# Performance work log

Hardware: AMD Instinct MI355X
Metric: run time of the kernel (lower is better)

The kernel has to match this reference:

```python
import jax, jax.numpy as jnp
import numpy as np

N_NODES = 100000
N_EDGES = 3200000
N_TYPES = 4
SIGMA = 0.05


def setup_inputs() -> dict:
    key = jax.random.key(0)
    k1, k2, k3, k4 = jax.random.split(key, 4)
    pos = jax.random.uniform(k1, (N_NODES, 2), dtype=jnp.float32)
    # per-type attraction-repulsion parameters (p0..p3), kept positive-ish
    p = jax.random.uniform(k2, (N_TYPES, 4), dtype=jnp.float32) + 0.2
    cell_type = jax.random.randint(k3, (N_NODES,), 0, N_TYPES, dtype=jnp.int32)
    edge_index = jax.random.randint(k4, (2, N_EDGES), 0, N_NODES, dtype=jnp.int32)
    # func_type[n] % 2 == 0 -> 'arbitrary' (f1), == 1 -> 'tanh' (f2)
    func_type = jnp.arange(N_TYPES, dtype=jnp.int32)
    return {"pos": pos, "p": p, "cell_type": cell_type,
            "edge_index": edge_index, "func_type": func_type}


def reference(pos, p, cell_type, edge_index, func_type):
    n_cells = pos.shape[0]
    inv_2s2 = 1.0 / (2.0 * SIGMA * SIGMA)

    src, dst = edge_index[1], edge_index[0]
    valid = src != dst  # remove_self_loops, done via masking for static shapes

    dpos = pos[src] - pos[dst]                  # [E, 2] bc_dpos = identity
    d2 = jnp.sum(dpos * dpos, axis=1)           # [E]
    d2 = jnp.where(valid, d2, 1.0)              # guard pow/sqrt/div at self-loops
    dist = jnp.sqrt(d2)

    params = p[cell_type[dst]]                  # [E, 4] gather per dst node type
    p0, p1, p2, p3 = params[:, 0], params[:, 1], params[:, 2], params[:, 3]

    # 'arbitrary' attraction-repulsion force
    f1 = p0 * jnp.exp(-(d2 ** p1) * inv_2s2) - p2 * jnp.exp(-(d2 ** p3) * inv_2s2)
    # 'tanh' force
    f2 = p0 * jnp.tanh((dist - p1) * p2) / dist

    is_tanh = (func_type[cell_type[dst]] % 2) == 1
    coef = jnp.where(is_tanh, f2, f1)           # [E]
    msg = coef[:, None] * dpos                  # field_j = 1 (has_field=False)
    msg = jnp.where(valid[:, None], msg, 0.0)

    sums = jax.ops.segment_sum(msg, dst, num_segments=n_cells)              # [N, 2]
    counts = jax.ops.segment_sum(valid.astype(pos.dtype), dst, num_segments=n_cells)
    return sums / jnp.maximum(counts, 1.0)[:, None]  # mean aggregation
```

## Files before the change

### kernel.cpp

```cpp
#include <hip/hip_runtime.h>

#define N_NODES 100000
#define N_EDGES 3200000

#define BLOCK   256
#define BLOCKB  512
#define WPB     8
#define NBLK    1280
#define EB      (N_EDGES / NBLK)
#define KAIT    10
#define KATAIL  (EB - 9 * BLOCK)
#define CSHIFT  11
#define CHUNK   2048
#define NCHUNK  49
#define CAP     128
#define BPC     16
#define BACT    (NCHUNK * BPC)
#define NSEG    (NBLK / BPC)
#define SRC_BITS 17
#define SRC_MASK ((1u << SRC_BITS) - 1)

#define FP_SCALE 131072.0f
#define FP_BIAS  (1 << 18)
#define FLD_MASK ((1u << 26) - 1)

__device__ __forceinline__ float edge_coef(float d2, float4 pp, int ct) {
    if (ct & 1) {
        const float dist = sqrtf(d2);
        const float x = (dist - pp.y) * pp.z;
        const float e = __expf(2.0f * x);
        const float t = (e - 1.0f) / (e + 1.0f);
        return pp.x * t / dist;
    }
    const float l = __logf(d2);
    const float a = __expf(pp.y * l);
    const float b = __expf(pp.w * l);
    return pp.x * __expf(-200.0f * a) - pp.z * __expf(-200.0f * b);
}

__global__ __launch_bounds__(BLOCK) void kA_scatter(
    const int* __restrict__ edge_index,
    unsigned int* __restrict__ bucket,
    unsigned int* __restrict__ cnts)
{
    __shared__ unsigned int cnt[NCHUNK];
    __shared__ unsigned int offs[NCHUNK];
    __shared__ unsigned int cur[NCHUNK];
    __shared__ unsigned int ordered[EB];
    const int g = blockIdx.x, tid = threadIdx.x;
    const int lane = tid & 63, wid = tid >> 6;
    if (tid < NCHUNK) cnt[tid] = 0u;
    __syncthreads();
    const int* __restrict__ dstRow = edge_index;
    const int* __restrict__ srcRow = edge_index + N_EDGES;
    const int e0 = g * EB + tid;
    const bool tailok = tid < KATAIL;
    int dv[KAIT], sv[KAIT];
    #pragma unroll
    for (int k = 0; k < KAIT; ++k) {
        if (k < 9 || tailok)
            dv[k] = __builtin_nontemporal_load(&dstRow[e0 + k * BLOCK]);
        else dv[k] = -1;
    }
    #pragma unroll
    for (int k = 0; k < KAIT; ++k) {
        if (k < 9 || tailok)
            sv[k] = __builtin_nontemporal_load(&srcRow[e0 + k * BLOCK]);
        else sv[k] = 0;
    }
    #pragma unroll
    for (int k = 0; k < KAIT; ++k)
        if (dv[k] >= 0) atomicAdd(&cnt[dv[k] >> CSHIFT], 1u);
    __syncthreads();
    if (tid == 0) {
        unsigned int run = 0u;
        for (int c = 0; c < NCHUNK; ++c) { offs[c] = run; run += cnt[c]; }
    }
    if (tid < NCHUNK) cur[tid] = 0u;
    __syncthreads();
    #pragma unroll
    for (int k = 0; k < KAIT; ++k) {
        const int d = dv[k];
        if (d >= 0) {
            const int c = d >> CSHIFT;
            const unsigned int rec =
                ((unsigned int)(d & (CHUNK - 1)) << SRC_BITS)
                | (unsigned int)sv[k];
            const unsigned int slot = atomicAdd(&cur[c], 1u);
            ordered[offs[c] + slot] = rec;
        }
    }
    __syncthreads();
    unsigned int* __restrict__ myseg = bucket + (size_t)g * NCHUNK * CAP;
    for (int c = wid; c < NCHUNK; c += 4) {
        const unsigned int n = min(cnt[c], (unsigned)CAP);
        const unsigned int o = offs[c];
        for (unsigned int i = lane; i < n; i += 64u)
            myseg[(unsigned)c * CAP + i] = ordered[o + i];
    }
    if (tid < NCHUNK) cnts[tid * NBLK + g] = min(cnt[tid], (unsigned)CAP);
}

__global__ __launch_bounds__(BLOCKB) void kB_accum(
    const float* __restrict__ pos,
    const float* __restrict__ p,
    const int*   __restrict__ cell_type,
    const unsigned int* __restrict__ bucket,
    const unsigned int* __restrict__ cnts,
    unsigned long long* __restrict__ partials)
{
    __shared__ unsigned long long acc[CHUNK];
    __shared__ unsigned int      pc[CHUNK];
    __shared__ float4            ptab[4];
    const int g = blockIdx.x, tid = threadIdx.x;
    const int lane = tid & 63, wid = tid >> 6;
    const int c   = g / BPC;
    const int sub = g - c * BPC;
    const int lo  = c * CHUNK;
    if (tid < 4) ptab[tid] = ((const float4*)p)[tid];
    for (int i = tid; i < CHUNK; i += BLOCKB) {
        acc[i] = 0ull;
        const int gi = lo + i;
        unsigned int w = 0u;
        if (gi < N_NODES) {
            const float2 pd = ((const float2*)pos)[gi];
            unsigned int qx = (unsigned int)__float2int_rn(pd.x * 32768.0f);
            unsigned int qy = (unsigned int)__float2int_rn(pd.y * 32768.0f);
            qx = min(qx, 32767u);
            qy = min(qy, 32767u);
            w = (qx << 17) | (qy << 2) | ((unsigned int)cell_type[gi] & 3u);
        }
        pc[i] = w;
    }
    __syncthreads();

#define PROCESS_REC(rec, psv)                                               \
    {                                                                       \
        const int dl = (int)((rec) >> SRC_BITS);                            \
        const unsigned int w = pc[dl];                                      \
        const float pdx = (float)(w >> 17) * (1.0f / 32768.0f);             \
        const float pdy = (float)((w >> 2) & 0x7FFFu) * (1.0f / 32768.0f);  \
        const int ct = (int)(w & 3u);                                       \
        const float dx = (psv).x - pdx;                                     \
        const float dy = (psv).y - pdy;                                     \
        const float d2 = dx * dx + dy * dy;                                 \
        const float4 pp = ptab[ct];                                         \
        const float coef = edge_coef(d2, pp, ct);                           \
        const int fx = __float2int_rn(coef * dx * FP_SCALE);                \
        const int fy = __float2int_rn(coef * dy * FP_SCALE);                \
        atomicAdd(&acc[dl],                                                 \
              (1ull << 52)                                                  \
            | ((unsigned long long)(unsigned)(fx + FP_BIAS) << 26)          \
            |  (unsigned long long)(unsigned)(fy + FP_BIAS));               \
    }

    const int segbase = sub * NSEG + wid;
    unsigned int nn[10]; unsigned int rc[10];
    #pragma unroll
    for (int k = 0; k < 10; ++k)
        nn[k] = cnts[c * NBLK + segbase + WPB * k];
    #pragma unroll
    for (int k = 0; k < 10; ++k)
        rc[k] = __builtin_nontemporal_load(
            bucket + ((size_t)(segbase + WPB * k) * NCHUNK + c) * CAP + lane);

    bool v[10]; float2 ps[10];
#define GATH(k)                                                             \
    {                                                                       \
        v[k] = (unsigned)lane < nn[k];                                      \
        if (v[k]) {                                                         \
            const int s = (int)(rc[k] & SRC_MASK);                          \
            if (s == lo + (int)(rc[k] >> SRC_BITS)) v[k] = false;   \
            else ps[k] = ((const float2*)pos)[s];                           \
        }                                                                   \
    }
#define COMP(k) { if (v[k]) PROCESS_REC(rc[k], ps[k]); }
    GATH(0) GATH(1) GATH(2) GATH(3)
    COMP(0) GATH(4)
    COMP(1) GATH(5)
    COMP(2) GATH(6)
    COMP(3) GATH(7)
    COMP(4) GATH(8)
    COMP(5) GATH(9)
    COMP(6) COMP(7) COMP(8) COMP(9)
#undef GATH
#undef COMP

    #pragma unroll
    for (int k = 0; k < 10; ++k) {
        const bool v2 = (unsigned)(64 + lane) < nn[k];
        if (__any(v2)) {
            if (v2) {
                const unsigned int r = __builtin_nontemporal_load(
                    bucket + ((size_t)(segbase + WPB * k) * NCHUNK + c) * CAP
                    + 64 + lane);
                const int s = (int)(r & SRC_MASK);
                if (s != lo + (int)(r >> SRC_BITS)) {
                    const float2 psv = ((const float2*)pos)[s];
                    PROCESS_REC(r, psv);
                }
            }
        }
    }
#undef PROCESS_REC
    __syncthreads();
    unsigned long long* dp = partials + (size_t)g * CHUNK;
    for (int i = tid; i < CHUNK; i += BLOCKB) dp[i] = acc[i];
}

__global__ __launch_bounds__(BLOCK) void kC_final(
    const unsigned long long* __restrict__ partials,
    float* __restrict__ out)
{
    const int i = blockIdx.x * BLOCK + threadIdx.x;
    if (i >= N_NODES) return;
    const int c  = i >> CSHIFT;
    const int il = i & (CHUNK - 1);
    const unsigned long long* b = partials + ((size_t)c * BPC) * CHUNK + il;
    unsigned long long v = 0ull;
    #pragma unroll
    for (int s = 0; s < BPC; ++s) v += b[(size_t)s * CHUNK];
    const unsigned  n  = (unsigned)(v >> 52);
    const long long ex = (long long)((v >> 26) & FLD_MASK);
    const long long ey = (long long)(v & FLD_MASK);
    const float sx = (float)(ex - (long long)n * FP_BIAS) * (1.0f / FP_SCALE);
    const float sy = (float)(ey - (long long)n * FP_BIAS) * (1.0f / FP_SCALE);
    const float cc = (float)(n > 1u ? n : 1u);
    float2 r;
    r.x = sx / cc;
    r.y = sy / cc;
    ((float2*)out)[i] = r;
}

__global__ __launch_bounds__(BLOCK) void edge_kernel_atomic(
    const float* __restrict__ pos, const float* __restrict__ p,
    const int* __restrict__ cell_type, const int* __restrict__ edge_index,
    unsigned long long* __restrict__ acc)
{
    const int e = blockIdx.x * blockDim.x + threadIdx.x;
    if (e >= N_EDGES) return;
    const int d = edge_index[e];
    const int s = edge_index[N_EDGES + e];
    if (s == d) return;
    const float2 ps = ((const float2*)pos)[s];
    const float2 pd = ((const float2*)pos)[d];
    const float dx = ps.x - pd.x;
    const float dy = ps.y - pd.y;
    const float d2 = dx * dx + dy * dy;
    const int ct = cell_type[d];
    const float4 pp = ((const float4*)p)[ct];
    const float coef = edge_coef(d2, pp, ct);
    const int fx = __float2int_rn(coef * dx * FP_SCALE);
    const int fy = __float2int_rn(coef * dy * FP_SCALE);
    atomicAdd(&acc[d],
          (1ull << 52)
        | ((unsigned long long)(unsigned)(fx + FP_BIAS) << 26)
        |  (unsigned long long)(unsigned)(fy + FP_BIAS));
}

__global__ __launch_bounds__(BLOCK) void finalize_flat_kernel(
    const unsigned long long* __restrict__ acc, float* __restrict__ out)
{
    const int i = blockIdx.x * BLOCK + threadIdx.x;
    if (i >= N_NODES) return;
    const unsigned long long v = acc[i];
    const unsigned  n  = (unsigned)(v >> 52);
    const long long ex = (long long)((v >> 26) & FLD_MASK);
    const long long ey = (long long)(v & FLD_MASK);
    const float sx = (float)(ex - (long long)n * FP_BIAS) * (1.0f / FP_SCALE);
    const float sy = (float)(ey - (long long)n * FP_BIAS) * (1.0f / FP_SCALE);
    const float cc = (float)(n > 1u ? n : 1u);
    float2 r;
    r.x = sx / cc;
    r.y = sy / cc;
    ((float2*)out)[i] = r;
}

extern "C" void kernel_launch(void* const* d_in, const int* in_sizes, int n_in,
                              void* d_out, int out_size, void* d_ws, size_t ws_size,
                              hipStream_t stream) {
    const float* pos        = (const float*)d_in[0];
    const float* p          = (const float*)d_in[1];
    const int*   cell_type  = (const int*)d_in[2];
    const int*   edge_index = (const int*)d_in[3];
    float* out = (float*)d_out;

    const size_t bucket_bytes   = (size_t)NBLK * NCHUNK * CAP * 4;
    const size_t partials_bytes = (size_t)BACT * CHUNK * 8;
    const size_t cnts_bytes     = (size_t)NCHUNK * NBLK * 4;
    const size_t need = bucket_bytes + partials_bytes + cnts_bytes;

    if (ws_size >= need) {
        unsigned int* bucket = (unsigned int*)d_ws;
        unsigned long long* partials =
            (unsigned long long*)((char*)d_ws + bucket_bytes);
        unsigned int* cnts =
            (unsigned int*)((char*)d_ws + bucket_bytes + partials_bytes);

        kA_scatter<<<NBLK, BLOCK, 0, stream>>>(edge_index, bucket, cnts);
        kB_accum  <<<BACT, BLOCKB, 0, stream>>>(pos, p, cell_type, bucket,
                                                cnts, partials);
        kC_final  <<<(N_NODES + BLOCK - 1) / BLOCK, BLOCK, 0, stream>>>(
            partials, out);
    } else {
        unsigned long long* acc = (unsigned long long*)d_ws;
        (void)hipMemsetAsync(d_ws, 0,
                             (size_t)N_NODES * sizeof(unsigned long long), stream);
        edge_kernel_atomic<<<(N_EDGES + 255) / 256, 256, 0, stream>>>(
            pos, p, cell_type, edge_index, acc);
        finalize_flat_kernel<<<(N_NODES + 255) / 256, 256, 0, stream>>>(acc, out);
    }
}
```

Baseline: 115.6 us.

## Double bucketing blocks, halve bucket capacity, use wave-scan for chunk offsets

Doubles the number of bucketing blocks so each handles half as many edges, and halves the per-segment bucket capacity to 64 so every segment fits one wavefront load. The consumer kernel now processes segments in two batches of ten instead of one batch plus an overflow pass for records beyond 64. The serial prefix sum over chunk counts is replaced with a wavefront shuffle scan. The aim is more parallelism in the bucketing pass and no divergent overflow loop, at the cost of more segment metadata and a tighter capacity that could overflow if a segment gets more than 64 edges.

```diff
diff --git a/kernel.cpp b/kernel.cpp
--- a/kernel.cpp
+++ b/kernel.cpp
@@ -6,14 +6,14 @@
 #define BLOCK   256
 #define BLOCKB  512
 #define WPB     8
-#define NBLK    1280
+#define NBLK    2560
 #define EB      (N_EDGES / NBLK)
-#define KAIT    10
-#define KATAIL  (EB - 9 * BLOCK)
+#define KAIT    5
+#define KATAIL  (EB - 4 * BLOCK)
 #define CSHIFT  11
 #define CHUNK   2048
 #define NCHUNK  49
-#define CAP     128
+#define CAP     64
 #define BPC     16
 #define BACT    (NCHUNK * BPC)
 #define NSEG    (NBLK / BPC)
@@ -58,13 +58,13 @@
     int dv[KAIT], sv[KAIT];
     #pragma unroll
     for (int k = 0; k < KAIT; ++k) {
-        if (k < 9 || tailok)
+        if (k < 4 || tailok)
             dv[k] = __builtin_nontemporal_load(&dstRow[e0 + k * BLOCK]);
         else dv[k] = -1;
     }
     #pragma unroll
     for (int k = 0; k < KAIT; ++k) {
-        if (k < 9 || tailok)
+        if (k < 4 || tailok)
             sv[k] = __builtin_nontemporal_load(&srcRow[e0 + k * BLOCK]);
         else sv[k] = 0;
     }
@@ -72,9 +72,15 @@
     for (int k = 0; k < KAIT; ++k)
         if (dv[k] >= 0) atomicAdd(&cnt[dv[k] >> CSHIFT], 1u);
     __syncthreads();
-    if (tid == 0) {
-        unsigned int run = 0u;
-        for (int c = 0; c < NCHUNK; ++c) { offs[c] = run; run += cnt[c]; }
+    if (wid == 0) {
+        unsigned int x = (lane < NCHUNK) ? cnt[lane] : 0u;
+        const unsigned int own = x;
+        #pragma unroll
+        for (int off = 1; off < 64; off <<= 1) {
+            const unsigned int y = __shfl_up(x, off, 64);
+            if (lane >= off) x += y;
+        }
+        if (lane < NCHUNK) offs[lane] = x - own;
     }
     if (tid < NCHUNK) cur[tid] = 0u;
     __syncthreads();
@@ -154,17 +160,6 @@
             |  (unsigned long long)(unsigned)(fy + FP_BIAS));               \
     }
 
-    const int segbase = sub * NSEG + wid;
-    unsigned int nn[10]; unsigned int rc[10];
-    #pragma unroll
-    for (int k = 0; k < 10; ++k)
-        nn[k] = cnts[c * NBLK + segbase + WPB * k];
-    #pragma unroll
-    for (int k = 0; k < 10; ++k)
-        rc[k] = __builtin_nontemporal_load(
-            bucket + ((size_t)(segbase + WPB * k) * NCHUNK + c) * CAP + lane);
-
-    bool v[10]; float2 ps[10];
 #define GATH(k)                                                             \
     {                                                                       \
         v[k] = (unsigned)lane < nn[k];                                      \
@@ -175,33 +170,35 @@
         }                                                                   \
     }
 #define COMP(k) { if (v[k]) PROCESS_REC(rc[k], ps[k]); }
-    GATH(0) GATH(1) GATH(2) GATH(3)
-    COMP(0) GATH(4)
-    COMP(1) GATH(5)
-    COMP(2) GATH(6)
-    COMP(3) GATH(7)
-    COMP(4) GATH(8)
-    COMP(5) GATH(9)
-    COMP(6) COMP(7) COMP(8) COMP(9)
+
+    const int segbase = sub * NSEG + wid;
+#define RUNBATCH(B0)                                                        \
+    {                                                                       \
+        unsigned int nn[10]; unsigned int rc[10];                           \
+        bool v[10]; float2 ps[10];                                          \
+        _Pragma("unroll")                                                   \
+        for (int k = 0; k < 10; ++k)                                        \
+            nn[k] = cnts[c * NBLK + segbase + WPB * ((B0) + k)];            \
+        _Pragma("unroll")                                                   \
+        for (int k = 0; k < 10; ++k)                                        \
+            rc[k] = __builtin_nontemporal_load(                             \
+                bucket + ((size_t)(segbase + WPB * ((B0) + k)) * NCHUNK + c)\
+                * CAP + lane);                                              \
+        GATH(0) GATH(1) GATH(2) GATH(3)                                     \
+        COMP(0) GATH(4)                                                     \
+        COMP(1) GATH(5)                                                     \
+        COMP(2) GATH(6)                                                     \
+        COMP(3) GATH(7)                                                     \
+        COMP(4) GATH(8)                                                     \
+        COMP(5) GATH(9)                                                     \
+        COMP(6) COMP(7) COMP(8) COMP(9)                                     \
+    }
+
+    RUNBATCH(0)
+    RUNBATCH(10)
+#undef RUNBATCH
 #undef GATH
 #undef COMP
-
-    #pragma unroll
-    for (int k = 0; k < 10; ++k) {
-        const bool v2 = (unsigned)(64 + lane) < nn[k];
-        if (__any(v2)) {
-            if (v2) {
-                const unsigned int r = __builtin_nontemporal_load(
-                    bucket + ((size_t)(segbase + WPB * k) * NCHUNK + c) * CAP
-                    + 64 + lane);
-                const int s = (int)(r & SRC_MASK);
-                if (s != lo + (int)(r >> SRC_BITS)) {
-                    const float2 psv = ((const float2*)pos)[s];
-                    PROCESS_REC(r, psv);
-                }
-            }
-        }
-    }
 #undef PROCESS_REC
     __syncthreads();
     unsigned long long* dp = partials + (size_t)g * CHUNK;
```

Result: slower. 126.5 us (+9.4%).

## Scatter directly into fixed-capacity shared bins and filter self-loops in scatter

Applied to the files above, without the earlier changes.

The scatter kernel now drops its count, prefix-sum and compacted-reorder passes. Each edge claims a slot in a fixed 128-wide per-chunk shared bin with one atomic, which removes two barriers and a serial scan. Self-loop filtering moves from the accumulate kernel into the scatter, so self-loops never take bucket slots and the gather loop loses a compare. The edge coefficient math now uses raw AMDGCN exp2/log/rcp/sqrt intrinsics with folded log2e constants. The flat copy-out loop visits all 49*128 slots per block, so it does wasted iterations, and the changed intrinsics may cost some accuracy.

```diff
diff --git a/kernel.cpp b/kernel.cpp
--- a/kernel.cpp
+++ b/kernel.cpp
@@ -14,6 +14,7 @@
 #define CHUNK   2048
 #define NCHUNK  49
 #define CAP     128
+#define CAPSH   7
 #define BPC     16
 #define BACT    (NCHUNK * BPC)
 #define NSEG    (NBLK / BPC)
@@ -24,18 +25,21 @@
 #define FP_BIAS  (1 << 18)
 #define FLD_MASK ((1u << 26) - 1)
 
+#define TWO_LOG2E   2.885390082f
+#define N200_LOG2E -288.5390082f
+
 __device__ __forceinline__ float edge_coef(float d2, float4 pp, int ct) {
     if (ct & 1) {
-        const float dist = sqrtf(d2);
+        const float dist = __builtin_amdgcn_sqrtf(d2);
         const float x = (dist - pp.y) * pp.z;
-        const float e = __expf(2.0f * x);
-        const float t = (e - 1.0f) / (e + 1.0f);
-        return pp.x * t / dist;
-    }
-    const float l = __logf(d2);
-    const float a = __expf(pp.y * l);
-    const float b = __expf(pp.w * l);
-    return pp.x * __expf(-200.0f * a) - pp.z * __expf(-200.0f * b);
+        const float e = __builtin_amdgcn_exp2f(TWO_LOG2E * x);
+        return pp.x * (e - 1.0f) * __builtin_amdgcn_rcpf((e + 1.0f) * dist);
+    }
+    const float L = __builtin_amdgcn_logf(d2);
+    const float a = __builtin_amdgcn_exp2f(pp.y * L);
+    const float b = __builtin_amdgcn_exp2f(pp.w * L);
+    return pp.x * __builtin_amdgcn_exp2f(N200_LOG2E * a)
+         - pp.z * __builtin_amdgcn_exp2f(N200_LOG2E * b);
 }
 
 __global__ __launch_bounds__(BLOCK) void kA_scatter(
@@ -44,11 +48,8 @@
     unsigned int* __restrict__ cnts)
 {
     __shared__ unsigned int cnt[NCHUNK];
-    __shared__ unsigned int offs[NCHUNK];
-    __shared__ unsigned int cur[NCHUNK];
-    __shared__ unsigned int ordered[EB];
+    __shared__ unsigned int seg[NCHUNK * CAP];
     const int g = blockIdx.x, tid = threadIdx.x;
-    const int lane = tid & 63, wid = tid >> 6;
     if (tid < NCHUNK) cnt[tid] = 0u;
     __syncthreads();
     const int* __restrict__ dstRow = edge_index;
@@ -70,14 +71,7 @@
     }
     #pragma unroll
     for (int k = 0; k < KAIT; ++k)
-        if (dv[k] >= 0) atomicAdd(&cnt[dv[k] >> CSHIFT], 1u);
-    __syncthreads();
-    if (tid == 0) {
-        unsigned int run = 0u;
-        for (int c = 0; c < NCHUNK; ++c) { offs[c] = run; run += cnt[c]; }
-    }
-    if (tid < NCHUNK) cur[tid] = 0u;
-    __syncthreads();
+        if (dv[k] == sv[k]) dv[k] = -1;
     #pragma unroll
     for (int k = 0; k < KAIT; ++k) {
         const int d = dv[k];
@@ -86,17 +80,19 @@
             const unsigned int rec =
                 ((unsigned int)(d & (CHUNK - 1)) << SRC_BITS)
                 | (unsigned int)sv[k];
-            const unsigned int slot = atomicAdd(&cur[c], 1u);
-            ordered[offs[c] + slot] = rec;
+            const unsigned int slot = atomicAdd(&cnt[c], 1u);
+            if (slot < CAP)
+                seg[((unsigned)c << CAPSH) + slot] = rec;
         }
     }
     __syncthreads();
     unsigned int* __restrict__ myseg = bucket + (size_t)g * NCHUNK * CAP;
-    for (int c = wid; c < NCHUNK; c += 4) {
+    for (int j = tid; j < NCHUNK * CAP; j += BLOCK) {
+        const int c = j >> CAPSH;
+        const unsigned int idx = (unsigned int)(j & (CAP - 1));
         const unsigned int n = min(cnt[c], (unsigned)CAP);
-        const unsigned int o = offs[c];
-        for (unsigned int i = lane; i < n; i += 64u)
-            myseg[(unsigned)c * CAP + i] = ordered[o + i];
+        if (idx < n)
+            myseg[j] = seg[j];
     }
     if (tid < NCHUNK) cnts[tid * NBLK + g] = min(cnt[tid], (unsigned)CAP);
 }
@@ -168,11 +164,8 @@
 #define GATH(k)                                                             \
     {                                                                       \
         v[k] = (unsigned)lane < nn[k];                                      \
-        if (v[k]) {                                                         \
-            const int s = (int)(rc[k] & SRC_MASK);                          \
-            if (s == lo + (int)(rc[k] >> SRC_BITS)) v[k] = false;   \
-            else ps[k] = ((const float2*)pos)[s];                           \
-        }                                                                   \
+        if (v[k])                                                           \
+            ps[k] = ((const float2*)pos)[(int)(rc[k] & SRC_MASK)];          \
     }
 #define COMP(k) { if (v[k]) PROCESS_REC(rc[k], ps[k]); }
     GATH(0) GATH(1) GATH(2) GATH(3)
@@ -194,11 +187,8 @@
                 const unsigned int r = __builtin_nontemporal_load(
                     bucket + ((size_t)(segbase + WPB * k) * NCHUNK + c) * CAP
                     + 64 + lane);
-                const int s = (int)(r & SRC_MASK);
-                if (s != lo + (int)(r >> SRC_BITS)) {
-                    const float2 psv = ((const float2*)pos)[s];
-                    PROCESS_REC(r, psv);
-                }
+                const float2 psv = ((const float2*)pos)[(int)(r & SRC_MASK)];
+                PROCESS_REC(r, psv);
             }
         }
     }
```

New measurement: 113.5 us. About the same (-1.8%).
